# Kernel tuning notes

Measured on AMD Instinct MI355X. Metric: run time of the kernel, lower is better.

Reference implementation:

```python
import jax, jax.numpy as jnp
import numpy as np

GRID = 52
NUM_BOXES = 2
NUM_CLASSES = 5
LAMBDA_COORD = 5.0
LAMBDA_CONF = 1.0
LAMBDA_CLASS = 1.0
ALPHA = 0.25
GAMMA = 2.0
CH = NUM_BOXES * (5 + NUM_CLASSES)  # 20
B = 256


def setup_inputs() -> dict:
    key = jax.random.key(0)
    k1, k2 = jax.random.split(key)
    predictions = jax.random.normal(k1, (B, GRID, GRID, CH), dtype=jnp.float32)
    targets = jax.random.uniform(k2, (B, GRID, GRID, CH), dtype=jnp.float32)
    return {"predictions": predictions, "targets": targets}


def _focal_elementwise(logits, t):
    # stable BCE-with-logits, elementwise
    ce = jnp.maximum(logits, 0.0) - logits * t + jnp.log1p(jnp.exp(-jnp.abs(logits)))
    p = jax.nn.sigmoid(logits)
    p_t = p * t + (1.0 - p) * (1.0 - t)
    alpha_t = ALPHA * t + (1.0 - ALPHA) * (1.0 - t)
    return alpha_t * (1.0 - p_t) ** GAMMA * ce


def reference(predictions, targets):
    nb5 = NUM_BOXES * 5
    # [B, S, S, num_boxes, 5]
    pred_box = predictions[..., :nb5].reshape(B, GRID, GRID, NUM_BOXES, 5)
    tgt_box = targets[..., :nb5].reshape(B, GRID, GRID, NUM_BOXES, 5)

    pred_conf = pred_box[..., 4]  # [B,S,S,NB]
    tgt_conf = tgt_box[..., 4]
    has_obj = (tgt_conf > 0.5).astype(predictions.dtype)  # [B,S,S,NB]
    num_objects = jnp.maximum(jnp.sum(has_obj), 1.0)

    # confidence: per-scalar focal (reduction='mean' on a single element == element)
    conf_loss = jnp.sum(_focal_elementwise(pred_conf, tgt_conf)) / B

    # coordinates: masked sum of squared errors over x,y,w,h
    sq = jnp.sum((pred_box[..., :4] - tgt_box[..., :4]) ** 2, axis=-1)  # [B,S,S,NB]
    coord_loss = jnp.sum(has_obj * sq) / B

    # classification: CE per cell, counted once per object box in that cell
    pred_cls = predictions[..., nb5:nb5 + NUM_CLASSES]  # [B,S,S,C]
    tgt_idx = jnp.argmax(targets[..., nb5:nb5 + NUM_CLASSES], axis=-1)  # [B,S,S]
    logp = jax.nn.log_softmax(pred_cls, axis=-1)
    nll = -jnp.take_along_axis(logp, tgt_idx[..., None], axis=-1)[..., 0]  # [B,S,S]
    obj_count = jnp.sum(has_obj, axis=-1)  # [B,S,S] number of object boxes per cell
    class_loss = jnp.sum(obj_count * nll) / num_objects

    total_loss = LAMBDA_COORD * coord_loss + LAMBDA_CONF * conf_loss + LAMBDA_CLASS * class_loss
    return total_loss
```

## Files before the change

### kernel.cpp

```cpp
#include <hip/hip_runtime.h>


constexpr int   kB        = 256;
constexpr int   kGrid     = 52;
constexpr int   kCells    = kB * kGrid * kGrid;
constexpr int   kBlocks   = kCells / 256;
constexpr float kAlpha    = 0.25f;
constexpr float kLamCoord = 5.0f;

#define AS1(p) ((const __attribute__((address_space(1))) void*)(p))
#define AS3(p) ((__attribute__((address_space(3))) void*)(p))

__global__ __launch_bounds__(256) void phobia_main_kernel(
    const float4* __restrict__ pred4,
    const float4* __restrict__ tgt4,
    float4* __restrict__ part)
{
    __shared__ float4 lds[4][640];

    const int tid  = threadIdx.x;
    const int wave = tid >> 6;
    const int lane = tid & 63;
    const size_t base4 = (size_t)blockIdx.x * 1280 + (size_t)wave * 320;

    #pragma unroll
    for (int k = 0; k < 5; ++k) {
        __builtin_amdgcn_global_load_lds(AS1(pred4 + base4 + k * 64 + lane),
                                         AS3(&lds[wave][k * 64]), 16, 0, 0);
        __builtin_amdgcn_global_load_lds(AS1(tgt4  + base4 + k * 64 + lane),
                                         AS3(&lds[wave][320 + k * 64]), 16, 0, 0);
    }
    asm volatile("s_waitcnt vmcnt(0)" ::: "memory");
    __builtin_amdgcn_sched_barrier(0);

    const float4 P0 = lds[wave][lane * 5 + 0], P1 = lds[wave][lane * 5 + 1];
    const float4 P2 = lds[wave][lane * 5 + 2], P3 = lds[wave][lane * 5 + 3];
    const float4 T0 = lds[wave][320 + lane * 5 + 0], T1 = lds[wave][320 + lane * 5 + 1];
    const float4 T2 = lds[wave][320 + lane * 5 + 2], T3 = lds[wave][320 + lane * 5 + 3];

    const float p[16] = {P0.x, P0.y, P0.z, P0.w,  P1.x, P1.y, P1.z, P1.w,
                         P2.x, P2.y, P2.z, P2.w,  P3.x, P3.y, P3.z, P3.w};
    const float t[16] = {T0.x, T0.y, T0.z, T0.w,  T1.x, T1.y, T1.z, T1.w,
                         T2.x, T2.y, T2.z, T2.w,  T3.x, T3.y, T3.z, T3.w};

    float coord = 0.f, conf = 0.f;
    float obj_count = 0.f;
    #pragma unroll
    for (int n = 0; n < 2; ++n) {
        const int b5    = n * 5;
        const float l   = p[b5 + 4];
        const float tc  = t[b5 + 4];
        const float has = (tc > 0.5f) ? 1.f : 0.f;

        float sq = 0.f;
        #pragma unroll
        for (int k = 0; k < 4; ++k) {
            const float d = p[b5 + k] - t[b5 + k];
            sq += d * d;
        }
        coord += has * sq;

        const float ce = fmaxf(l, 0.f) - l * tc + log1pf(__expf(-fabsf(l)));
        const float s  = 1.f / (1.f + __expf(-l));
        const float pt = s * tc + (1.f - s) * (1.f - tc);
        const float at = kAlpha * tc + (1.f - kAlpha) * (1.f - tc);
        const float om = 1.f - pt;
        conf += at * om * om * ce;

        obj_count += has;
    }

    float bv = t[10], pv = p[10];
    if (t[11] > bv) { bv = t[11]; pv = p[11]; }
    if (t[12] > bv) { bv = t[12]; pv = p[12]; }
    if (t[13] > bv) { bv = t[13]; pv = p[13]; }
    if (t[14] > bv) { bv = t[14]; pv = p[14]; }

    const float m  = fmaxf(fmaxf(fmaxf(p[10], p[11]), fmaxf(p[12], p[13])), p[14]);
    const float se = __expf(p[10] - m) + __expf(p[11] - m) + __expf(p[12] - m)
                   + __expf(p[13] - m) + __expf(p[14] - m);
    float cls  = obj_count * (__logf(se) + m - pv);
    float nobj = obj_count;

    #pragma unroll
    for (int off = 32; off >= 1; off >>= 1) {
        coord += __shfl_down(coord, off);
        conf  += __shfl_down(conf,  off);
        cls   += __shfl_down(cls,   off);
        nobj  += __shfl_down(nobj,  off);
    }

    if (lane == 0) {
        float4 o; o.x = coord; o.y = conf; o.z = cls; o.w = nobj;
        lds[wave][0] = o;
    }
    __syncthreads();
    if (tid == 0) {
        const float4 a = lds[0][0], b = lds[1][0], c = lds[2][0], d = lds[3][0];
        float4 o;
        o.x = a.x + b.x + c.x + d.x;
        o.y = a.y + b.y + c.y + d.y;
        o.z = a.z + b.z + c.z + d.z;
        o.w = a.w + b.w + c.w + d.w;
        part[blockIdx.x] = o;
    }
}

__global__ __launch_bounds__(256) void phobia_reduce_kernel(
    const float4* __restrict__ part, float* __restrict__ out)
{
    const int tid = threadIdx.x;
    float c0 = 0.f, c1 = 0.f, c2 = 0.f, c3 = 0.f;
    for (int i = tid; i < kBlocks; i += 256) {
        const float4 v = part[i];
        c0 += v.x; c1 += v.y; c2 += v.z; c3 += v.w;
    }
    #pragma unroll
    for (int off = 32; off >= 1; off >>= 1) {
        c0 += __shfl_down(c0, off);
        c1 += __shfl_down(c1, off);
        c2 += __shfl_down(c2, off);
        c3 += __shfl_down(c3, off);
    }
    __shared__ float sred[4][4];
    const int wave = tid >> 6;
    const int lane = tid & 63;
    if (lane == 0) {
        sred[wave][0] = c0; sred[wave][1] = c1;
        sred[wave][2] = c2; sred[wave][3] = c3;
    }
    __syncthreads();
    if (tid == 0) {
        const float coord = sred[0][0] + sred[1][0] + sred[2][0] + sred[3][0];
        const float conf  = sred[0][1] + sred[1][1] + sred[2][1] + sred[3][1];
        const float cls   = sred[0][2] + sred[1][2] + sred[2][2] + sred[3][2];
        const float nobj  = sred[0][3] + sred[1][3] + sred[2][3] + sred[3][3];
        out[0] = kLamCoord * (coord / (float)kB)
               + (conf / (float)kB)
               + cls / fmaxf(nobj, 1.f);
    }
}

extern "C" void kernel_launch(void* const* d_in, const int* in_sizes, int n_in,
                              void* d_out, int out_size, void* d_ws, size_t ws_size,
                              hipStream_t stream) {
    const float4* pred4 = (const float4*)d_in[0];
    const float4* tgt4  = (const float4*)d_in[1];
    float4* part = (float4*)d_ws;
    float* out = (float*)d_out;

    phobia_main_kernel<<<kBlocks, 256, 0, stream>>>(pred4, tgt4, part);
    phobia_reduce_kernel<<<1, 256, 0, stream>>>(part, out);
}
```

Measured before the change: 27.17 us.

## Persistent waves with double-buffered LDS prefetch of cell chunks

Replaces the one-chunk-per-wave launch with 512 persistent blocks whose waves loop over chunks with a grid stride. Each wave prefetches the next chunk into a second LDS buffer while it computes the current one. The goal is to overlap memory latency with compute, cut block launch overhead and shrink the partial-sum array. The cost is double the LDS per block, which lowers occupancy, and load imbalance in the tail.

```diff
diff --git a/kernel.cpp b/kernel.cpp
--- a/kernel.cpp
+++ b/kernel.cpp
@@ -4,83 +4,108 @@
 constexpr int   kB        = 256;
 constexpr int   kGrid     = 52;
 constexpr int   kCells    = kB * kGrid * kGrid;
-constexpr int   kBlocks   = kCells / 256;
+constexpr int   kChunks   = kCells / 64;
+constexpr int   kBlocksM  = 512;
+constexpr int   kWaves    = kBlocksM * 4;
 constexpr float kAlpha    = 0.25f;
 constexpr float kLamCoord = 5.0f;
 
 #define AS1(p) ((const __attribute__((address_space(1))) void*)(p))
 #define AS3(p) ((__attribute__((address_space(3))) void*)(p))
 
+__device__ __forceinline__ void issue_chunk_loads(const float4* __restrict__ pred4,
+                                                  const float4* __restrict__ tgt4,
+                                                  int chunk, float4* dst, int lane)
+{
+    const size_t b4 = (size_t)chunk * 320;
+    #pragma unroll
+    for (int k = 0; k < 5; ++k) {
+        __builtin_amdgcn_global_load_lds(AS1(pred4 + b4 + k * 64 + lane),
+                                         AS3(dst + k * 64), 16, 0, 0);
+        __builtin_amdgcn_global_load_lds(AS1(tgt4  + b4 + k * 64 + lane),
+                                         AS3(dst + 320 + k * 64), 16, 0, 0);
+    }
+}
+
 __global__ __launch_bounds__(256) void phobia_main_kernel(
     const float4* __restrict__ pred4,
     const float4* __restrict__ tgt4,
     float4* __restrict__ part)
 {
-    __shared__ float4 lds[4][640];
+    __shared__ float4 lds[4][2][640];
 
-    const int tid  = threadIdx.x;
-    const int wave = tid >> 6;
-    const int lane = tid & 63;
-    const size_t base4 = (size_t)blockIdx.x * 1280 + (size_t)wave * 320;
+    const int tid   = threadIdx.x;
+    const int wave  = tid >> 6;
+    const int lane  = tid & 63;
+    const int gwave = blockIdx.x * 4 + wave;
 
-    #pragma unroll
-    for (int k = 0; k < 5; ++k) {
-        __builtin_amdgcn_global_load_lds(AS1(pred4 + base4 + k * 64 + lane),
-                                         AS3(&lds[wave][k * 64]), 16, 0, 0);
-        __builtin_amdgcn_global_load_lds(AS1(tgt4  + base4 + k * 64 + lane),
-                                         AS3(&lds[wave][320 + k * 64]), 16, 0, 0);
+    float coord = 0.f, conf = 0.f, cls = 0.f, nobj = 0.f;
+
+    int cur = gwave;
+    int buf = 0;
+    issue_chunk_loads(pred4, tgt4, cur, &lds[wave][0][0], lane);
+    int next = cur + kWaves;
+
+    while (cur < kChunks) {
+        if (next < kChunks) {
+            issue_chunk_loads(pred4, tgt4, next, &lds[wave][buf ^ 1][0], lane);
+            asm volatile("s_waitcnt vmcnt(10)" ::: "memory");
+        } else {
+            asm volatile("s_waitcnt vmcnt(0)" ::: "memory");
+        }
+        __builtin_amdgcn_sched_barrier(0);
+
+        const float4* L = &lds[wave][buf][0];
+        const float4 P0 = L[lane * 5 + 0], P1 = L[lane * 5 + 1];
+        const float4 P2 = L[lane * 5 + 2], P3 = L[lane * 5 + 3];
+        const float4 T0 = L[320 + lane * 5 + 0], T1 = L[320 + lane * 5 + 1];
+        const float4 T2 = L[320 + lane * 5 + 2], T3 = L[320 + lane * 5 + 3];
+
+        const float p[16] = {P0.x, P0.y, P0.z, P0.w,  P1.x, P1.y, P1.z, P1.w,
+                             P2.x, P2.y, P2.z, P2.w,  P3.x, P3.y, P3.z, P3.w};
+        const float t[16] = {T0.x, T0.y, T0.z, T0.w,  T1.x, T1.y, T1.z, T1.w,
+                             T2.x, T2.y, T2.z, T2.w,  T3.x, T3.y, T3.z, T3.w};
+
+        float obj_count = 0.f;
+        #pragma unroll
+        for (int n = 0; n < 2; ++n) {
+            const int b5    = n * 5;
+            const float l   = p[b5 + 4];
+            const float tc  = t[b5 + 4];
+            const float has = (tc > 0.5f) ? 1.f : 0.f;
+
+            float sq = 0.f;
+            #pragma unroll
+            for (int k = 0; k < 4; ++k) {
+                const float d = p[b5 + k] - t[b5 + k];
+                sq += d * d;
+            }
+            coord += has * sq;
+
+            const float ce = fmaxf(l, 0.f) - l * tc + log1pf(__expf(-fabsf(l)));
+            const float s  = 1.f / (1.f + __expf(-l));
+            const float pt = s * tc + (1.f - s) * (1.f - tc);
+            const float at = kAlpha * tc + (1.f - kAlpha) * (1.f - tc);
+            const float om = 1.f - pt;
+            conf += at * om * om * ce;
+
+            obj_count += has;
+        }
+        nobj += obj_count;
+
+        float bv = t[10], pv = p[10];
+        if (t[11] > bv) { bv = t[11]; pv = p[11]; }
+        if (t[12] > bv) { bv = t[12]; pv = p[12]; }
+        if (t[13] > bv) { bv = t[13]; pv = p[13]; }
+        if (t[14] > bv) { bv = t[14]; pv = p[14]; }
+
+        const float m  = fmaxf(fmaxf(fmaxf(p[10], p[11]), fmaxf(p[12], p[13])), p[14]);
+        const float se = __expf(p[10] - m) + __expf(p[11] - m) + __expf(p[12] - m)
+                       + __expf(p[13] - m) + __expf(p[14] - m);
+        cls += obj_count * (__logf(se) + m - pv);
+
+        cur = next; next += kWaves; buf ^= 1;
     }
-    asm volatile("s_waitcnt vmcnt(0)" ::: "memory");
-    __builtin_amdgcn_sched_barrier(0);
-
-    const float4 P0 = lds[wave][lane * 5 + 0], P1 = lds[wave][lane * 5 + 1];
-    const float4 P2 = lds[wave][lane * 5 + 2], P3 = lds[wave][lane * 5 + 3];
-    const float4 T0 = lds[wave][320 + lane * 5 + 0], T1 = lds[wave][320 + lane * 5 + 1];
-    const float4 T2 = lds[wave][320 + lane * 5 + 2], T3 = lds[wave][320 + lane * 5 + 3];
-
-    const float p[16] = {P0.x, P0.y, P0.z, P0.w,  P1.x, P1.y, P1.z, P1.w,
-                         P2.x, P2.y, P2.z, P2.w,  P3.x, P3.y, P3.z, P3.w};
-    const float t[16] = {T0.x, T0.y, T0.z, T0.w,  T1.x, T1.y, T1.z, T1.w,
-                         T2.x, T2.y, T2.z, T2.w,  T3.x, T3.y, T3.z, T3.w};
-
-    float coord = 0.f, conf = 0.f;
-    float obj_count = 0.f;
-    #pragma unroll
-    for (int n = 0; n < 2; ++n) {
-        const int b5    = n * 5;
-        const float l   = p[b5 + 4];
-        const float tc  = t[b5 + 4];
-        const float has = (tc > 0.5f) ? 1.f : 0.f;
-
-        float sq = 0.f;
-        #pragma unroll
-        for (int k = 0; k < 4; ++k) {
-            const float d = p[b5 + k] - t[b5 + k];
-            sq += d * d;
-        }
-        coord += has * sq;
-
-        const float ce = fmaxf(l, 0.f) - l * tc + log1pf(__expf(-fabsf(l)));
-        const float s  = 1.f / (1.f + __expf(-l));
-        const float pt = s * tc + (1.f - s) * (1.f - tc);
-        const float at = kAlpha * tc + (1.f - kAlpha) * (1.f - tc);
-        const float om = 1.f - pt;
-        conf += at * om * om * ce;
-
-        obj_count += has;
-    }
-
-    float bv = t[10], pv = p[10];
-    if (t[11] > bv) { bv = t[11]; pv = p[11]; }
-    if (t[12] > bv) { bv = t[12]; pv = p[12]; }
-    if (t[13] > bv) { bv = t[13]; pv = p[13]; }
-    if (t[14] > bv) { bv = t[14]; pv = p[14]; }
-
-    const float m  = fmaxf(fmaxf(fmaxf(p[10], p[11]), fmaxf(p[12], p[13])), p[14]);
-    const float se = __expf(p[10] - m) + __expf(p[11] - m) + __expf(p[12] - m)
-                   + __expf(p[13] - m) + __expf(p[14] - m);
-    float cls  = obj_count * (__logf(se) + m - pv);
-    float nobj = obj_count;
 
     #pragma unroll
     for (int off = 32; off >= 1; off >>= 1) {
@@ -92,11 +117,12 @@
 
     if (lane == 0) {
         float4 o; o.x = coord; o.y = conf; o.z = cls; o.w = nobj;
-        lds[wave][0] = o;
+        lds[wave][0][0] = o;
     }
     __syncthreads();
     if (tid == 0) {
-        const float4 a = lds[0][0], b = lds[1][0], c = lds[2][0], d = lds[3][0];
+        const float4 a = lds[0][0][0], b = lds[1][0][0];
+        const float4 c = lds[2][0][0], d = lds[3][0][0];
         float4 o;
         o.x = a.x + b.x + c.x + d.x;
         o.y = a.y + b.y + c.y + d.y;
@@ -111,8 +137,9 @@
 {
     const int tid = threadIdx.x;
     float c0 = 0.f, c1 = 0.f, c2 = 0.f, c3 = 0.f;
-    for (int i = tid; i < kBlocks; i += 256) {
-        const float4 v = part[i];
+    #pragma unroll
+    for (int r = 0; r < kBlocksM / 256; ++r) {
+        const float4 v = part[r * 256 + tid];
         c0 += v.x; c1 += v.y; c2 += v.z; c3 += v.w;
     }
     #pragma unroll
@@ -149,6 +176,6 @@
     float4* part = (float4*)d_ws;
     float* out = (float*)d_out;
 
-    phobia_main_kernel<<<kBlocks, 256, 0, stream>>>(pred4, tgt4, part);
+    phobia_main_kernel<<<kBlocksM, 256, 0, stream>>>(pred4, tgt4, part);
     phobia_reduce_kernel<<<1, 256, 0, stream>>>(part, out);
 }
```

New measurement: 26.57 us. 1.02x faster.
